# Kernel tuning notes

Hardware: AMD Instinct MI355X
Metric: run time of the kernel (lower is better)

The kernel has to match this reference:

```python
import jax, jax.numpy as jnp
import numpy as np

BATCH, T, IN, OUT, H = 16, 4096, 256, 256, 512


def setup_inputs() -> dict:
    key = jax.random.key(0)
    ks = jax.random.split(key, 8)
    gB = float(np.sqrt(6.0 / (H + IN)))   # glorot uniform bound for B (out_axis=0,in_axis=1)
    gC = float(np.sqrt(6.0 / (OUT + H)))
    gD = float(np.sqrt(6.0 / (OUT + IN)))
    return {
        "X": jax.random.normal(ks[0], (BATCH, T, IN), dtype=jnp.float32),
        "nu_log": jax.random.uniform(ks[1], (H,), dtype=jnp.float32),
        "theta_log": jax.random.uniform(ks[2], (H,), dtype=jnp.float32),
        "B_re": jax.random.uniform(ks[3], (H, IN), jnp.float32, -gB, gB),
        "B_im": jax.random.uniform(ks[4], (H, IN), jnp.float32, -gB, gB),
        "C_re": jax.random.uniform(ks[5], (OUT, H), jnp.float32, -gC, gC),
        "C_im": jax.random.uniform(ks[6], (OUT, H), jnp.float32, -gC, gC),
        "D": jax.random.uniform(ks[7], (OUT, IN), jnp.float32, -gD, gD),
        "bh_re": jnp.zeros((H,), jnp.float32),
        "bh_im": jnp.zeros((H,), jnp.float32),
        "bias_output": jnp.zeros((OUT,), jnp.float32),
    }


def reference(X, nu_log, theta_log, B_re, B_im, C_re, C_im, D, bh_re, bh_im, bias_output):
    # lambda = exp(-exp(nu_log) + i*exp(theta_log)); gamma = sqrt(1-|lambda|^2)
    lam = jnp.exp(-jnp.exp(nu_log) + 1j * jnp.exp(theta_log))          # [H] complex64
    gamma = jnp.sqrt(1.0 - jnp.abs(lam) ** 2)                           # [H] float32
    Bc = (B_re + 1j * B_im).astype(jnp.complex64)
    Cc = (C_re + 1j * C_im).astype(jnp.complex64)
    bh = (bh_re + 1j * bh_im).astype(jnp.complex64)

    # Input projection into hidden space (note: original adds bias_hidden here AND inside the scan step)
    u = gamma * (jnp.einsum('bti,hi->bth', X.astype(jnp.complex64), Bc) + bh)  # [B,T,H] complex64

    def step(h, u_t):
        h = lam * h + u_t + bh
        return h, h

    h0 = jnp.zeros((X.shape[0], lam.shape[0]), dtype=jnp.complex64)
    h_N, ys = jax.lax.scan(step, h0, jnp.swapaxes(u, 0, 1))             # ys: [T,B,H]

    Y = jnp.real(jnp.einsum('tbh,oh->bto', ys, Cc))                     # [B,T,OUT]
    Y = Y + jnp.einsum('bti,oi->bto', X, D) + bias_output
    return (Y, h_N)
```

## Files before the change

kernel.cpp:

```cpp
#include <hip/hip_runtime.h>
#include <math.h>


#define T_LEN  4096
#define NBATCH 16
#define IN_D   256
#define OUT_D  256
#define HID    512
#define M_TOT  65536

typedef __attribute__((ext_vector_type(8))) short short8;
typedef __attribute__((ext_vector_type(4))) float float4v;

static __device__ __forceinline__ unsigned short f2bf(float f) {
    union { float f; unsigned u; } v; v.f = f;
    unsigned r = v.u + 0x7FFFu + ((v.u >> 16) & 1u);
    return (unsigned short)(r >> 16);
}
static __device__ __forceinline__ float bf2f(unsigned short h) {
    union { unsigned u; float f; } v; v.u = ((unsigned)h) << 16;
    return v.f;
}


__global__ __launch_bounds__(256) void cvt_x(const float* __restrict__ X,
                                             unsigned short* __restrict__ Xbf)
{
    int e = (blockIdx.x * 256 + threadIdx.x) * 4;
    float4 v = *(const float4*)(X + e);
    ushort4 o;
    o.x = f2bf(v.x); o.y = f2bf(v.y); o.z = f2bf(v.z); o.w = f2bf(v.w);
    *(ushort4*)(Xbf + e) = o;
}

__global__ __launch_bounds__(256) void cvt_w(
    const float* __restrict__ B_re, const float* __restrict__ B_im,
    const float* __restrict__ C_re, const float* __restrict__ C_im,
    const float* __restrict__ Dm, unsigned short* __restrict__ W)
{
    int e = (blockIdx.x * 256 + threadIdx.x) * 4;
    const float* src; int off;
    if (e < 262144) {
        if (e < 131072) { src = B_re; off = e; }
        else            { src = B_im; off = e - 131072; }
    } else {
        int e2 = e - 262144;
        int row = e2 / 1280, c = e2 % 1280;
        if      (c < 512)  { src = C_re; off = row * 512 + c; }
        else if (c < 1024) { src = C_im; off = row * 512 + c - 512; }
        else               { src = Dm;   off = row * 256 + c - 1024; }
    }
    float4 v = *(const float4*)(src + off);
    ushort4 o;
    o.x = f2bf(v.x); o.y = f2bf(v.y); o.z = f2bf(v.z); o.w = f2bf(v.w);
    *(ushort4*)(W + e) = o;
}

__global__ __launch_bounds__(256) void lam_prep(
    const float* __restrict__ nu_log, const float* __restrict__ theta_log,
    const float* __restrict__ bh_re, float4* __restrict__ Ltab)
{
    int ch = blockIdx.x * 256 + threadIdx.x;
    if (ch >= HID) return;
    float mod = expf(-expf(nu_log[ch]));
    float th  = expf(theta_log[ch]);
    Ltab[ch] = make_float4(mod * cosf(th), mod * sinf(th),
                           sqrtf(fmaxf(0.f, 1.f - mod * mod)), bh_re[ch]);
}

__global__ __launch_bounds__(256, 3) void gemm_scan(
    const unsigned short* __restrict__ Xbf, const unsigned short* __restrict__ Bw,
    const float4* __restrict__ Ltab, const float* __restrict__ bh_im,
    unsigned short* __restrict__ Hbuf, float* __restrict__ hN, int hN_mode)
{
    __shared__ unsigned short smem[160 * 136];

    const int tid  = threadIdx.x;
    const int lane = tid & 63;
    const int wv   = tid >> 6;
    const int wr   = wv >> 1, wc = wv & 1;
    const int col  = lane & 15, quad = lane >> 4;

    const int bid  = blockIdx.x;
    const int xcd  = bid & 7;
    const int idx  = bid >> 3;
    const int chg  = idx & 7;
    const int bc   = xcd * 64 + (idx >> 3);
    const int b    = bc >> 5;
    const int cIdx = bc & 31;

    const int mBase = b * T_LEN + cIdx * 128 - 32;
    const int bLo   = b * T_LEN;

    float4v acc[20];
#pragma unroll
    for (int i = 0; i < 20; ++i) acc[i] = (float4v)0.f;

    int arow[5];
#pragma unroll
    for (int mt = 0; mt < 5; ++mt) {
        int gm = mBase + wr * 80 + mt * 16 + col;
        arow[mt] = gm < bLo ? bLo : gm;
    }
    const unsigned short* Br = Bw + (size_t)(wc * 512 + chg * 64 + col) * IN_D + quad * 8;

#pragma unroll
    for (int ks = 0; ks < 8; ++ks) {
        short8 af[5], bf[4];
#pragma unroll
        for (int mt = 0; mt < 5; ++mt)
            af[mt] = *(const short8*)(Xbf + (size_t)arow[mt] * IN_D + quad * 8 + ks * 32);
#pragma unroll
        for (int nt = 0; nt < 4; ++nt)
            bf[nt] = *(const short8*)(Br + nt * 16 * IN_D + ks * 32);
#pragma unroll
        for (int mt = 0; mt < 5; ++mt)
#pragma unroll
            for (int nt = 0; nt < 4; ++nt)
                acc[mt * 4 + nt] = __builtin_amdgcn_mfma_f32_16x16x32_bf16(
                    af[mt], bf[nt], acc[mt * 4 + nt], 0, 0, 0);
    }

#pragma unroll
    for (int nt = 0; nt < 4; ++nt) {
        const int chl = nt * 16 + col;
        float4 L = Ltab[chg * 64 + chl];
        const float gam = L.z;
        const float bv  = wc ? bh_im[chg * 64 + chl] : L.w;
        const int   cl  = wc * 64 + chl;
#pragma unroll
        for (int mt = 0; mt < 5; ++mt)
#pragma unroll
            for (int r = 0; r < 4; ++r) {
                const int ml = wr * 80 + mt * 16 + quad * 4 + r;
                smem[ml * 136 + cl] = f2bf(gam * (acc[mt * 4 + nt][r] + bv));
            }
    }
    __syncthreads();

    if (wv == 0) {
        float4 L = Ltab[chg * 64 + lane];
        const float lre = L.x, lim = L.y, bre = L.w;
        const float bim = bh_im[chg * 64 + lane];
        float hre = 0.f, him = 0.f;
        const int s0 = (cIdx == 0) ? 32 : 0;
        for (int t0 = s0; t0 < 160; t0 += 8) {
            float ur[8], ui[8];
#pragma unroll
            for (int s = 0; s < 8; ++s) {
                ur[s] = bf2f(smem[(t0 + s) * 136 + lane]);
                ui[s] = bf2f(smem[(t0 + s) * 136 + 64 + lane]);
            }
#pragma unroll
            for (int s = 0; s < 8; ++s) {
                float nr = lre * hre - lim * him + ur[s] + bre;
                him      = lre * him + lim * hre + ui[s] + bim;
                hre = nr;
                smem[(t0 + s) * 136 + lane]      = f2bf(hre);
                smem[(t0 + s) * 136 + 64 + lane] = f2bf(-him);
            }
        }
        if (hN_mode && cIdx == 31) {
            const int ch = chg * 64 + lane;
            if (hN_mode == 2) {
                hN[((size_t)b * HID + ch) * 2]     = hre;
                hN[((size_t)b * HID + ch) * 2 + 1] = him;
            } else {
                hN[(size_t)b * HID + ch] = hre;
            }
        }
    }
    __syncthreads();

    const int p  = tid >> 7;
    const int t7 = tid & 127;
    const int rg = t7 >> 3;
    const int l8 = t7 & 7;
    unsigned short* Hp = Hbuf + ((size_t)(p * 8 + chg) * M_TOT
                                 + (size_t)(b * T_LEN + cIdx * 128)) * 64;
#pragma unroll
    for (int it = 0; it < 8; ++it) {
        const int row = it * 16 + rg;
        short8 v = *(const short8*)(smem + (32 + row) * 136 + p * 64 + l8 * 8);
        *(short8*)(Hp + row * 64 + l8 * 8) = v;
    }
}

__global__ __launch_bounds__(256, 3) void gemm_c(
    const unsigned short* __restrict__ Hbuf, const unsigned short* __restrict__ Xbf,
    const unsigned short* __restrict__ W2,
    const float* __restrict__ bias_out, float* __restrict__ Y)
{
    __shared__ unsigned short sA[128 * 68];
    __shared__ unsigned short sB[128 * 68];
    const int tid  = threadIdx.x;
    const int lane = tid & 63;
    const int wv   = tid >> 6;
    const int wr   = wv >> 1, wc = wv & 1;
    const int col  = lane & 15, quad = lane >> 4;

    const int bid  = blockIdx.x;
    const int xcd  = bid & 7;
    const int idx  = bid >> 3;
    const int Mblk = xcd * 64 + (idx >> 1);
    const int Nblk = idx & 1;
    const int m0 = Mblk * 128, o0 = Nblk * 128;

    float4v acc[16];
#pragma unroll
    for (int i = 0; i < 16; ++i) acc[i] = (float4v)0.f;

    short8 ra[4], rb[4];
#pragma unroll
    for (int i = 0; i < 4; ++i) {
        int cid = i * 256 + tid;
        int r = cid >> 3, c8 = cid & 7;
        ra[i] = *(const short8*)(Hbuf + (size_t)(m0 + r) * 64 + c8 * 8);
        rb[i] = *(const short8*)(W2 + (size_t)(o0 + r) * 1280 + c8 * 8);
    }
    for (int k0 = 0; k0 < 20; ++k0) {
        __syncthreads();
#pragma unroll
        for (int i = 0; i < 4; ++i) {
            int cid = i * 256 + tid;
            int r = cid >> 3, c8 = cid & 7;
            *(short8*)(sA + r * 68 + c8 * 8) = ra[i];
            *(short8*)(sB + r * 68 + c8 * 8) = rb[i];
        }
        __syncthreads();
        if (k0 < 19) {
            const int kn = k0 + 1;
#pragma unroll
            for (int i = 0; i < 4; ++i) {
                int cid = i * 256 + tid;
                int r = cid >> 3, c8 = cid & 7;
                if (kn < 16)
                    ra[i] = *(const short8*)(Hbuf + (size_t)kn * (M_TOT * 64)
                                             + (size_t)(m0 + r) * 64 + c8 * 8);
                else
                    ra[i] = *(const short8*)(Xbf + (size_t)(m0 + r) * 256
                                             + (kn - 16) * 64 + c8 * 8);
                rb[i] = *(const short8*)(W2 + (size_t)(o0 + r) * 1280 + kn * 64 + c8 * 8);
            }
        }
#pragma unroll
        for (int kk = 0; kk < 2; ++kk) {
            short8 af[4], bf[4];
#pragma unroll
            for (int mt = 0; mt < 4; ++mt)
                af[mt] = *(const short8*)(sA + (wr * 64 + mt * 16 + col) * 68 + kk * 32 + quad * 8);
#pragma unroll
            for (int nt = 0; nt < 4; ++nt)
                bf[nt] = *(const short8*)(sB + (wc * 64 + nt * 16 + col) * 68 + kk * 32 + quad * 8);
#pragma unroll
            for (int mt = 0; mt < 4; ++mt)
#pragma unroll
                for (int nt = 0; nt < 4; ++nt)
                    acc[mt * 4 + nt] = __builtin_amdgcn_mfma_f32_16x16x32_bf16(
                        af[mt], bf[nt], acc[mt * 4 + nt], 0, 0, 0);
        }
    }
#pragma unroll
    for (int nt = 0; nt < 4; ++nt) {
        const int o = o0 + wc * 64 + nt * 16 + col;
        const float bo = bias_out[o];
#pragma unroll
        for (int mt = 0; mt < 4; ++mt)
#pragma unroll
            for (int r = 0; r < 4; ++r) {
                const int m = m0 + wr * 64 + mt * 16 + quad * 4 + r;
                Y[(size_t)m * OUT_D + o] = acc[mt * 4 + nt][r] + bo;
            }
    }
}

extern "C" void kernel_launch(void* const* d_in, const int* in_sizes, int n_in,
                              void* d_out, int out_size, void* d_ws, size_t ws_size,
                              hipStream_t stream) {
    const float* X        = (const float*)d_in[0];
    const float* nu_log   = (const float*)d_in[1];
    const float* theta_lg = (const float*)d_in[2];
    const float* B_re     = (const float*)d_in[3];
    const float* B_im     = (const float*)d_in[4];
    const float* C_re     = (const float*)d_in[5];
    const float* C_im     = (const float*)d_in[6];
    const float* Dm       = (const float*)d_in[7];
    const float* bh_re    = (const float*)d_in[8];
    const float* bh_im    = (const float*)d_in[9];
    const float* bias_out = (const float*)d_in[10];

    float* Y = (float*)d_out;
    const int YSZ = NBATCH * T_LEN * OUT_D;
    int extra = out_size - YSZ;
    int mode = (extra >= NBATCH * HID * 2) ? 2 : ((extra >= NBATCH * HID) ? 1 : 0);
    float* hN = Y + YSZ;

    char* ws = (char*)d_ws;
    unsigned short* W    = (unsigned short*)ws;
    unsigned short* W2   = W + 262144;
    float4*         Ltab = (float4*)(ws + 1179648);
    unsigned short* Xbf  = (unsigned short*)(ws + 1187840);
    unsigned short* Hbuf = (unsigned short*)(ws + 34742272);

    cvt_x<<<dim3(16384), 256, 0, stream>>>(X, Xbf);
    cvt_w<<<dim3(576), 256, 0, stream>>>(B_re, B_im, C_re, C_im, Dm, W);
    lam_prep<<<dim3(2), 256, 0, stream>>>(nu_log, theta_lg, bh_re, Ltab);
    gemm_scan<<<dim3(4096), 256, 0, stream>>>(Xbf, W, Ltab, bh_im, Hbuf, hN, mode);
    gemm_c<<<dim3(1024), 256, 0, stream>>>(Hbuf, Xbf, W2, bias_out, Y);
}
```

Before: 360.6 us.

## Halve scan chunk length and use direct global-to-LDS loads in output GEMM

The fused GEMM+scan kernel now processes 64-step time chunks with a 16-step warm-up instead of 128 with 32. It launches twice as many blocks, uses less LDS and fewer accumulators, and raises the occupancy hint. The output GEMM drops its register-staged prefetch and loads tiles straight into LDS with global_load_lds into unpadded tiles. The extra blocks redo more warm-up recurrence and input-projection work, and the unpadded LDS rows plus the lost prefetch overlap may add bank conflicts and stalls.

```diff
diff --git a/kernel.cpp b/kernel.cpp
--- a/kernel.cpp
+++ b/kernel.cpp
@@ -20,6 +20,12 @@
 static __device__ __forceinline__ float bf2f(unsigned short h) {
     union { unsigned u; float f; } v; v.u = ((unsigned)h) << 16;
     return v.f;
+}
+
+static __device__ __forceinline__ void gl_lds16(const void* g, void* l) {
+    __builtin_amdgcn_global_load_lds(
+        (const __attribute__((address_space(1))) unsigned int*)g,
+        (__attribute__((address_space(3))) unsigned int*)l, 16, 0, 0);
 }
 
 
@@ -68,72 +74,74 @@
                            sqrtf(fmaxf(0.f, 1.f - mod * mod)), bh_re[ch]);
 }
 
-__global__ __launch_bounds__(256, 3) void gemm_scan(
+__global__ __launch_bounds__(256, 5) void gemm_scan(
     const unsigned short* __restrict__ Xbf, const unsigned short* __restrict__ Bw,
     const float4* __restrict__ Ltab, const float* __restrict__ bh_im,
     unsigned short* __restrict__ Hbuf, float* __restrict__ hN, int hN_mode)
 {
-    __shared__ unsigned short smem[160 * 136];
+    __shared__ unsigned short smem[80 * 136];
 
     const int tid  = threadIdx.x;
     const int lane = tid & 63;
     const int wv   = tid >> 6;
-    const int wr   = wv >> 1, wc = wv & 1;
     const int col  = lane & 15, quad = lane >> 4;
 
     const int bid  = blockIdx.x;
     const int xcd  = bid & 7;
     const int idx  = bid >> 3;
     const int chg  = idx & 7;
-    const int bc   = xcd * 64 + (idx >> 3);
-    const int b    = bc >> 5;
-    const int cIdx = bc & 31;
-
-    const int mBase = b * T_LEN + cIdx * 128 - 32;
+    const int bcI  = xcd * 128 + (idx >> 3);
+    const int b    = bcI >> 6;
+    const int cIdx = bcI & 63;
+
+    const int mBase = b * T_LEN + cIdx * 64 - 16;
     const int bLo   = b * T_LEN;
 
-    float4v acc[20];
-#pragma unroll
-    for (int i = 0; i < 20; ++i) acc[i] = (float4v)0.f;
+    float4v acc[10];
+#pragma unroll
+    for (int i = 0; i < 10; ++i) acc[i] = (float4v)0.f;
 
     int arow[5];
 #pragma unroll
     for (int mt = 0; mt < 5; ++mt) {
-        int gm = mBase + wr * 80 + mt * 16 + col;
+        int gm = mBase + mt * 16 + col;
         arow[mt] = gm < bLo ? bLo : gm;
     }
-    const unsigned short* Br = Bw + (size_t)(wc * 512 + chg * 64 + col) * IN_D + quad * 8;
+    const int pw = wv >> 1;
+    const int cb = (wv & 1) * 32;
+    const unsigned short* Br =
+        Bw + (size_t)(pw * 512 + chg * 64 + cb + col) * IN_D + quad * 8;
 
 #pragma unroll
     for (int ks = 0; ks < 8; ++ks) {
-        short8 af[5], bf[4];
+        short8 af[5], bf[2];
 #pragma unroll
         for (int mt = 0; mt < 5; ++mt)
             af[mt] = *(const short8*)(Xbf + (size_t)arow[mt] * IN_D + quad * 8 + ks * 32);
 #pragma unroll
-        for (int nt = 0; nt < 4; ++nt)
+        for (int nt = 0; nt < 2; ++nt)
             bf[nt] = *(const short8*)(Br + nt * 16 * IN_D + ks * 32);
 #pragma unroll
         for (int mt = 0; mt < 5; ++mt)
 #pragma unroll
-            for (int nt = 0; nt < 4; ++nt)
-                acc[mt * 4 + nt] = __builtin_amdgcn_mfma_f32_16x16x32_bf16(
-                    af[mt], bf[nt], acc[mt * 4 + nt], 0, 0, 0);
-    }
-
-#pragma unroll
-    for (int nt = 0; nt < 4; ++nt) {
-        const int chl = nt * 16 + col;
+            for (int nt = 0; nt < 2; ++nt)
+                acc[mt * 2 + nt] = __builtin_amdgcn_mfma_f32_16x16x32_bf16(
+                    af[mt], bf[nt], acc[mt * 2 + nt], 0, 0, 0);
+    }
+
+#pragma unroll
+    for (int nt = 0; nt < 2; ++nt) {
+        const int chl = cb + nt * 16 + col;
         float4 L = Ltab[chg * 64 + chl];
         const float gam = L.z;
-        const float bv  = wc ? bh_im[chg * 64 + chl] : L.w;
-        const int   cl  = wc * 64 + chl;
+        const float bv  = pw ? bh_im[chg * 64 + chl] : L.w;
+        const int   cl  = pw * 64 + chl;
 #pragma unroll
         for (int mt = 0; mt < 5; ++mt)
 #pragma unroll
             for (int r = 0; r < 4; ++r) {
-                const int ml = wr * 80 + mt * 16 + quad * 4 + r;
-                smem[ml * 136 + cl] = f2bf(gam * (acc[mt * 4 + nt][r] + bv));
+                const int ml = mt * 16 + quad * 4 + r;
+                smem[ml * 136 + cl] = f2bf(gam * (acc[mt * 2 + nt][r] + bv));
             }
     }
     __syncthreads();
@@ -143,8 +151,8 @@
         const float lre = L.x, lim = L.y, bre = L.w;
         const float bim = bh_im[chg * 64 + lane];
         float hre = 0.f, him = 0.f;
-        const int s0 = (cIdx == 0) ? 32 : 0;
-        for (int t0 = s0; t0 < 160; t0 += 8) {
+        const int s0 = (cIdx == 0) ? 16 : 0;
+        for (int t0 = s0; t0 < 80; t0 += 8) {
             float ur[8], ui[8];
 #pragma unroll
             for (int s = 0; s < 8; ++s) {
@@ -160,7 +168,7 @@
                 smem[(t0 + s) * 136 + 64 + lane] = f2bf(-him);
             }
         }
-        if (hN_mode && cIdx == 31) {
+        if (hN_mode && cIdx == 63) {
             const int ch = chg * 64 + lane;
             if (hN_mode == 2) {
                 hN[((size_t)b * HID + ch) * 2]     = hre;
@@ -177,27 +185,29 @@
     const int rg = t7 >> 3;
     const int l8 = t7 & 7;
     unsigned short* Hp = Hbuf + ((size_t)(p * 8 + chg) * M_TOT
-                                 + (size_t)(b * T_LEN + cIdx * 128)) * 64;
-#pragma unroll
-    for (int it = 0; it < 8; ++it) {
+                                 + (size_t)b * T_LEN + cIdx * 64) * 64;
+#pragma unroll
+    for (int it = 0; it < 4; ++it) {
         const int row = it * 16 + rg;
-        short8 v = *(const short8*)(smem + (32 + row) * 136 + p * 64 + l8 * 8);
+        short8 v = *(const short8*)(smem + (16 + row) * 136 + p * 64 + l8 * 8);
         *(short8*)(Hp + row * 64 + l8 * 8) = v;
     }
 }
 
-__global__ __launch_bounds__(256, 3) void gemm_c(
+__global__ __launch_bounds__(256, 4) void gemm_c(
     const unsigned short* __restrict__ Hbuf, const unsigned short* __restrict__ Xbf,
     const unsigned short* __restrict__ W2,
     const float* __restrict__ bias_out, float* __restrict__ Y)
 {
-    __shared__ unsigned short sA[128 * 68];
-    __shared__ unsigned short sB[128 * 68];
+    __shared__ unsigned short sA[128 * 64];
+    __shared__ unsigned short sB[128 * 64];
     const int tid  = threadIdx.x;
     const int lane = tid & 63;
     const int wv   = tid >> 6;
     const int wr   = wv >> 1, wc = wv & 1;
     const int col  = lane & 15, quad = lane >> 4;
+    const int lr   = lane >> 3;
+    const int lc   = lane & 7;
 
     const int bid  = blockIdx.x;
     const int xcd  = bid & 7;
@@ -210,48 +220,38 @@
 #pragma unroll
     for (int i = 0; i < 16; ++i) acc[i] = (float4v)0.f;
 
-    short8 ra[4], rb[4];
-#pragma unroll
-    for (int i = 0; i < 4; ++i) {
-        int cid = i * 256 + tid;
-        int r = cid >> 3, c8 = cid & 7;
-        ra[i] = *(const short8*)(Hbuf + (size_t)(m0 + r) * 64 + c8 * 8);
-        rb[i] = *(const short8*)(W2 + (size_t)(o0 + r) * 1280 + c8 * 8);
-    }
     for (int k0 = 0; k0 < 20; ++k0) {
         __syncthreads();
 #pragma unroll
-        for (int i = 0; i < 4; ++i) {
-            int cid = i * 256 + tid;
-            int r = cid >> 3, c8 = cid & 7;
-            *(short8*)(sA + r * 68 + c8 * 8) = ra[i];
-            *(short8*)(sB + r * 68 + c8 * 8) = rb[i];
+        for (int c = 0; c < 4; ++c) {
+            const int rr = wv * 32 + c * 8 + lr;
+            const unsigned short* ga;
+            if (k0 < 16)
+                ga = Hbuf + (size_t)k0 * (M_TOT * 64) + (size_t)(m0 + rr) * 64 + lc * 8;
+            else
+                ga = Xbf + (size_t)(m0 + rr) * 256 + (k0 - 16) * 64 + lc * 8;
+            gl_lds16(ga, sA + wv * 2048 + c * 512);
+        }
+#pragma unroll
+        for (int c = 0; c < 4; ++c) {
+            const int rr = wv * 32 + c * 8 + lr;
+            const unsigned short* gb =
+                W2 + (size_t)(o0 + rr) * 1280 + k0 * 64 + lc * 8;
+            gl_lds16(gb, sB + wv * 2048 + c * 512);
         }
         __syncthreads();
-        if (k0 < 19) {
-            const int kn = k0 + 1;
-#pragma unroll
-            for (int i = 0; i < 4; ++i) {
-                int cid = i * 256 + tid;
-                int r = cid >> 3, c8 = cid & 7;
-                if (kn < 16)
-                    ra[i] = *(const short8*)(Hbuf + (size_t)kn * (M_TOT * 64)
-                                             + (size_t)(m0 + r) * 64 + c8 * 8);
-                else
-                    ra[i] = *(const short8*)(Xbf + (size_t)(m0 + r) * 256
-                                             + (kn - 16) * 64 + c8 * 8);
-                rb[i] = *(const short8*)(W2 + (size_t)(o0 + r) * 1280 + kn * 64 + c8 * 8);
-            }
-        }
+
 #pragma unroll
         for (int kk = 0; kk < 2; ++kk) {
             short8 af[4], bf[4];
 #pragma unroll
             for (int mt = 0; mt < 4; ++mt)
-                af[mt] = *(const short8*)(sA + (wr * 64 + mt * 16 + col) * 68 + kk * 32 + quad * 8);
+                af[mt] = *(const short8*)(sA + (wr * 64 + mt * 16 + col) * 64
+                                          + kk * 32 + quad * 8);
 #pragma unroll
             for (int nt = 0; nt < 4; ++nt)
-                bf[nt] = *(const short8*)(sB + (wc * 64 + nt * 16 + col) * 68 + kk * 32 + quad * 8);
+                bf[nt] = *(const short8*)(sB + (wc * 64 + nt * 16 + col) * 64
+                                          + kk * 32 + quad * 8);
 #pragma unroll
             for (int mt = 0; mt < 4; ++mt)
 #pragma unroll
@@ -305,6 +305,6 @@
     cvt_x<<<dim3(16384), 256, 0, stream>>>(X, Xbf);
     cvt_w<<<dim3(576), 256, 0, stream>>>(B_re, B_im, C_re, C_im, Dm, W);
     lam_prep<<<dim3(2), 256, 0, stream>>>(nu_log, theta_lg, bh_re, Ltab);
-    gemm_scan<<<dim3(4096), 256, 0, stream>>>(Xbf, W, Ltab, bh_im, Hbuf, hN, mode);
+    gemm_scan<<<dim3(8192), 256, 0, stream>>>(Xbf, W, Ltab, bh_im, Hbuf, hN, mode);
     gemm_c<<<dim3(1024), 256, 0, stream>>>(Hbuf, Xbf, W2, bias_out, Y);
 }
```

Result: slower. 411.5 us (+14.1%).

## Double-buffer gemm_c via direct global-to-LDS loads with XOR swizzle; prefetch gemm_scan fragments

Applied to the files above, without the earlier changes.

gemm_c now streams A and B tiles straight into a two-stage LDS ring using global_load_lds, with an XOR swizzle in place of row padding. Loads are issued two stages ahead and synchronised with vmcnt waits and barriers, so the register round-trip and one of the two barriers per k-step are gone. gemm_scan register-prefetches the next k-slice of MFMA operands while the current one computes. Occupancy hints drop from 3 to 2 blocks per CU, trading occupancy for more registers and LDS, which risks less latency hiding.

```diff
diff --git a/kernel.cpp b/kernel.cpp
--- a/kernel.cpp
+++ b/kernel.cpp
@@ -20,6 +20,12 @@
 static __device__ __forceinline__ float bf2f(unsigned short h) {
     union { unsigned u; float f; } v; v.u = ((unsigned)h) << 16;
     return v.f;
+}
+
+static __device__ __forceinline__ void gl_lds16(const void* g, void* l) {
+    __builtin_amdgcn_global_load_lds(
+        (const __attribute__((address_space(1))) unsigned int*)g,
+        (__attribute__((address_space(3))) unsigned int*)l, 16, 0, 0);
 }
 
 
@@ -68,7 +74,7 @@
                            sqrtf(fmaxf(0.f, 1.f - mod * mod)), bh_re[ch]);
 }
 
-__global__ __launch_bounds__(256, 3) void gemm_scan(
+__global__ __launch_bounds__(256, 2) void gemm_scan(
     const unsigned short* __restrict__ Xbf, const unsigned short* __restrict__ Bw,
     const float4* __restrict__ Ltab, const float* __restrict__ bh_im,
     unsigned short* __restrict__ Hbuf, float* __restrict__ hN, int hN_mode)
@@ -104,22 +110,36 @@
     }
     const unsigned short* Br = Bw + (size_t)(wc * 512 + chg * 64 + col) * IN_D + quad * 8;
 
+#define LD_A(dst, ks)                                                          \
+    { _Pragma("unroll")                                                        \
+      for (int mt = 0; mt < 5; ++mt)                                           \
+          dst[mt] = *(const short8*)(Xbf + (size_t)arow[mt] * IN_D             \
+                                     + quad * 8 + (ks) * 32); }
+#define LD_B(dst, ks)                                                          \
+    { _Pragma("unroll")                                                        \
+      for (int nt = 0; nt < 4; ++nt)                                           \
+          dst[nt] = *(const short8*)(Br + nt * 16 * IN_D + (ks) * 32); }
+
+    short8 afC[5], bfC[4], afN[5], bfN[4];
+    LD_A(afC, 0) LD_B(bfC, 0)
 #pragma unroll
     for (int ks = 0; ks < 8; ++ks) {
-        short8 af[5], bf[4];
-#pragma unroll
-        for (int mt = 0; mt < 5; ++mt)
-            af[mt] = *(const short8*)(Xbf + (size_t)arow[mt] * IN_D + quad * 8 + ks * 32);
-#pragma unroll
-        for (int nt = 0; nt < 4; ++nt)
-            bf[nt] = *(const short8*)(Br + nt * 16 * IN_D + ks * 32);
+        if (ks < 7) { LD_A(afN, ks + 1) LD_B(bfN, ks + 1) }
 #pragma unroll
         for (int mt = 0; mt < 5; ++mt)
 #pragma unroll
             for (int nt = 0; nt < 4; ++nt)
                 acc[mt * 4 + nt] = __builtin_amdgcn_mfma_f32_16x16x32_bf16(
-                    af[mt], bf[nt], acc[mt * 4 + nt], 0, 0, 0);
-    }
+                    afC[mt], bfC[nt], acc[mt * 4 + nt], 0, 0, 0);
+        if (ks < 7) {
+#pragma unroll
+            for (int mt = 0; mt < 5; ++mt) afC[mt] = afN[mt];
+#pragma unroll
+            for (int nt = 0; nt < 4; ++nt) bfC[nt] = bfN[nt];
+        }
+    }
+#undef LD_A
+#undef LD_B
 
 #pragma unroll
     for (int nt = 0; nt < 4; ++nt) {
@@ -177,7 +197,7 @@
     const int rg = t7 >> 3;
     const int l8 = t7 & 7;
     unsigned short* Hp = Hbuf + ((size_t)(p * 8 + chg) * M_TOT
-                                 + (size_t)(b * T_LEN + cIdx * 128)) * 64;
+                                 + (size_t)b * T_LEN + cIdx * 128) * 64;
 #pragma unroll
     for (int it = 0; it < 8; ++it) {
         const int row = it * 16 + rg;
@@ -186,18 +206,21 @@
     }
 }
 
-__global__ __launch_bounds__(256, 3) void gemm_c(
+__global__ __launch_bounds__(256, 2) void gemm_c(
     const unsigned short* __restrict__ Hbuf, const unsigned short* __restrict__ Xbf,
     const unsigned short* __restrict__ W2,
     const float* __restrict__ bias_out, float* __restrict__ Y)
 {
-    __shared__ unsigned short sA[128 * 68];
-    __shared__ unsigned short sB[128 * 68];
+    __shared__ unsigned short sA[2][128 * 64];
+    __shared__ unsigned short sB[2][128 * 64];
     const int tid  = threadIdx.x;
     const int lane = tid & 63;
     const int wv   = tid >> 6;
     const int wr   = wv >> 1, wc = wv & 1;
     const int col  = lane & 15, quad = lane >> 4;
+    const int lr   = lane >> 3;
+    const int lc   = lane & 7;
+    const int lcS  = lc ^ lr;
 
     const int bid  = blockIdx.x;
     const int xcd  = bid & 7;
@@ -210,48 +233,52 @@
 #pragma unroll
     for (int i = 0; i < 16; ++i) acc[i] = (float4v)0.f;
 
-    short8 ra[4], rb[4];
-#pragma unroll
-    for (int i = 0; i < 4; ++i) {
-        int cid = i * 256 + tid;
-        int r = cid >> 3, c8 = cid & 7;
-        ra[i] = *(const short8*)(Hbuf + (size_t)(m0 + r) * 64 + c8 * 8);
-        rb[i] = *(const short8*)(W2 + (size_t)(o0 + r) * 1280 + c8 * 8);
-    }
+#define STAGE(p, k0)                                                           \
+    {                                                                          \
+        _Pragma("unroll")                                                      \
+        for (int c = 0; c < 4; ++c) {                                          \
+            const int rr = wv * 32 + c * 8 + lr;                               \
+            const unsigned short* ga;                                          \
+            if ((k0) < 16)                                                     \
+                ga = Hbuf + (size_t)(k0) * ((size_t)M_TOT * 64)                \
+                     + (size_t)(m0 + rr) * 64 + lcS * 8;                       \
+            else                                                               \
+                ga = Xbf + (size_t)(m0 + rr) * 256 + ((k0) - 16) * 64 + lcS * 8; \
+            gl_lds16(ga, &sA[p][wv * 2048 + c * 512]);                         \
+        }                                                                      \
+        _Pragma("unroll")                                                      \
+        for (int c = 0; c < 4; ++c) {                                          \
+            const int rr = wv * 32 + c * 8 + lr;                               \
+            gl_lds16(W2 + (size_t)(o0 + rr) * 1280 + (k0) * 64 + lcS * 8,      \
+                     &sB[p][wv * 2048 + c * 512]);                             \
+        }                                                                      \
+    }
+
+    STAGE(0, 0)
+    STAGE(1, 1)
+
     for (int k0 = 0; k0 < 20; ++k0) {
-        __syncthreads();
-#pragma unroll
-        for (int i = 0; i < 4; ++i) {
-            int cid = i * 256 + tid;
-            int r = cid >> 3, c8 = cid & 7;
-            *(short8*)(sA + r * 68 + c8 * 8) = ra[i];
-            *(short8*)(sB + r * 68 + c8 * 8) = rb[i];
-        }
-        __syncthreads();
-        if (k0 < 19) {
-            const int kn = k0 + 1;
-#pragma unroll
-            for (int i = 0; i < 4; ++i) {
-                int cid = i * 256 + tid;
-                int r = cid >> 3, c8 = cid & 7;
-                if (kn < 16)
-                    ra[i] = *(const short8*)(Hbuf + (size_t)kn * (M_TOT * 64)
-                                             + (size_t)(m0 + r) * 64 + c8 * 8);
-                else
-                    ra[i] = *(const short8*)(Xbf + (size_t)(m0 + r) * 256
-                                             + (kn - 16) * 64 + c8 * 8);
-                rb[i] = *(const short8*)(W2 + (size_t)(o0 + r) * 1280 + kn * 64 + c8 * 8);
-            }
-        }
+        const int p = k0 & 1;
+        if (k0 < 19) { asm volatile("s_waitcnt vmcnt(8)" ::: "memory"); }
+        else         { asm volatile("s_waitcnt vmcnt(0)" ::: "memory"); }
+        __builtin_amdgcn_s_barrier();
+        __builtin_amdgcn_sched_barrier(0);
+
 #pragma unroll
         for (int kk = 0; kk < 2; ++kk) {
             short8 af[4], bf[4];
 #pragma unroll
-            for (int mt = 0; mt < 4; ++mt)
-                af[mt] = *(const short8*)(sA + (wr * 64 + mt * 16 + col) * 68 + kk * 32 + quad * 8);
-#pragma unroll
-            for (int nt = 0; nt < 4; ++nt)
-                bf[nt] = *(const short8*)(sB + (wc * 64 + nt * 16 + col) * 68 + kk * 32 + quad * 8);
+            for (int mt = 0; mt < 4; ++mt) {
+                const int row = wr * 64 + mt * 16 + col;
+                af[mt] = *(const short8*)(&sA[p][(row * 64 + kk * 32 + quad * 8)
+                                                 ^ ((row & 7) << 3)]);
+            }
+#pragma unroll
+            for (int nt = 0; nt < 4; ++nt) {
+                const int row = wc * 64 + nt * 16 + col;
+                bf[nt] = *(const short8*)(&sB[p][(row * 64 + kk * 32 + quad * 8)
+                                                 ^ ((row & 7) << 3)]);
+            }
 #pragma unroll
             for (int mt = 0; mt < 4; ++mt)
 #pragma unroll
@@ -259,7 +286,14 @@
                     acc[mt * 4 + nt] = __builtin_amdgcn_mfma_f32_16x16x32_bf16(
                         af[mt], bf[nt], acc[mt * 4 + nt], 0, 0, 0);
         }
-    }
+
+        __builtin_amdgcn_sched_barrier(0);
+        __builtin_amdgcn_s_barrier();
+        __builtin_amdgcn_sched_barrier(0);
+        if (k0 < 18) STAGE(p, k0 + 2)
+    }
+#undef STAGE
+
 #pragma unroll
     for (int nt = 0; nt < 4; ++nt) {
         const int o = o0 + wc * 64 + nt * 16 + col;
```

Measured after the change: 397.7 us. +10.3%, slower.

## Fuse X conversion, input GEMM, chunked scan and output GEMM into one kernel

Applied to the files above, without the earlier changes.

Replaces the separate X conversion, gemm_scan and gemm_c kernels with a single kernel that converts a 96-row X tile to bf16 in shared memory, computes the B projection per 64-channel group, runs the truncated-warmup scan in LDS, and immediately accumulates the C and D projections into register-held Y tiles. This removes the global round trip of the bf16 X copy and the large hidden-state buffer, plus two launches. In exchange each block redoes the 32-step warmup window per channel group with 64-step chunks (more redundant GEMM and scan work), has lower occupancy, and the scan is split across four waves that each recompute a 32-step warmup.

```diff
diff --git a/kernel.cpp b/kernel.cpp
--- a/kernel.cpp
+++ b/kernel.cpp
@@ -8,6 +8,8 @@
 #define OUT_D  256
 #define HID    512
 #define M_TOT  65536
+#define XT_STR 264
+#define HT_STR 136
 
 typedef __attribute__((ext_vector_type(8))) short short8;
 typedef __attribute__((ext_vector_type(4))) float float4v;
@@ -22,16 +24,6 @@
     return v.f;
 }
 
-
-__global__ __launch_bounds__(256) void cvt_x(const float* __restrict__ X,
-                                             unsigned short* __restrict__ Xbf)
-{
-    int e = (blockIdx.x * 256 + threadIdx.x) * 4;
-    float4 v = *(const float4*)(X + e);
-    ushort4 o;
-    o.x = f2bf(v.x); o.y = f2bf(v.y); o.z = f2bf(v.z); o.w = f2bf(v.w);
-    *(ushort4*)(Xbf + e) = o;
-}
 
 __global__ __launch_bounds__(256) void cvt_w(
     const float* __restrict__ B_re, const float* __restrict__ B_im,
@@ -68,100 +60,128 @@
                            sqrtf(fmaxf(0.f, 1.f - mod * mod)), bh_re[ch]);
 }
 
-__global__ __launch_bounds__(256, 3) void gemm_scan(
-    const unsigned short* __restrict__ Xbf, const unsigned short* __restrict__ Bw,
+__global__ __launch_bounds__(256, 2) void lru_mega(
+    const float* __restrict__ X, const unsigned short* __restrict__ Bw,
+    const unsigned short* __restrict__ W2,
     const float4* __restrict__ Ltab, const float* __restrict__ bh_im,
-    unsigned short* __restrict__ Hbuf, float* __restrict__ hN, int hN_mode)
+    const float* __restrict__ bias_out,
+    float* __restrict__ Y, float* __restrict__ hN, int hN_mode)
 {
-    __shared__ unsigned short smem[160 * 136];
+    __shared__ unsigned short Xt[96 * XT_STR];
+    __shared__ unsigned short Ht[96 * HT_STR];
 
     const int tid  = threadIdx.x;
     const int lane = tid & 63;
     const int wv   = tid >> 6;
+    const int col  = lane & 15, quad = lane >> 4;
     const int wr   = wv >> 1, wc = wv & 1;
-    const int col  = lane & 15, quad = lane >> 4;
 
     const int bid  = blockIdx.x;
     const int xcd  = bid & 7;
-    const int idx  = bid >> 3;
-    const int chg  = idx & 7;
-    const int bc   = xcd * 64 + (idx >> 3);
-    const int b    = bc >> 5;
-    const int cIdx = bc & 31;
-
-    const int mBase = b * T_LEN + cIdx * 128 - 32;
-    const int bLo   = b * T_LEN;
-
-    float4v acc[20];
-#pragma unroll
-    for (int i = 0; i < 20; ++i) acc[i] = (float4v)0.f;
-
-    int arow[5];
-#pragma unroll
-    for (int mt = 0; mt < 5; ++mt) {
-        int gm = mBase + wr * 80 + mt * 16 + col;
-        arow[mt] = gm < bLo ? bLo : gm;
-    }
-    const unsigned short* Br = Bw + (size_t)(wc * 512 + chg * 64 + col) * IN_D + quad * 8;
-
-#pragma unroll
-    for (int ks = 0; ks < 8; ++ks) {
-        short8 af[5], bf[4];
-#pragma unroll
-        for (int mt = 0; mt < 5; ++mt)
-            af[mt] = *(const short8*)(Xbf + (size_t)arow[mt] * IN_D + quad * 8 + ks * 32);
-#pragma unroll
-        for (int nt = 0; nt < 4; ++nt)
-            bf[nt] = *(const short8*)(Br + nt * 16 * IN_D + ks * 32);
-#pragma unroll
-        for (int mt = 0; mt < 5; ++mt)
+    const int bc   = xcd * 128 + (bid >> 3);
+    const int b    = bc >> 6;
+    const int cIdx = bc & 63;
+    const int G0   = b * T_LEN + cIdx * 64;
+    const int bLo  = b * T_LEN;
+
+#pragma unroll 4
+    for (int i = 0; i < 24; ++i) {
+        const int r = wv * 24 + i;
+        int g = G0 - 32 + r; if (g < bLo) g = bLo;
+        float4 v = *(const float4*)(X + (size_t)g * IN_D + lane * 4);
+        ushort4 o;
+        o.x = f2bf(v.x); o.y = f2bf(v.y); o.z = f2bf(v.z); o.w = f2bf(v.w);
+        *(ushort4*)(Xt + r * XT_STR + lane * 4) = o;
+    }
+    __syncthreads();
+
+    float4v yac[16];
+#pragma unroll
+    for (int i = 0; i < 16; ++i) yac[i] = (float4v)0.f;
+
+    for (int p = 0; p < 8; ++p) {
+        float4v ua[12];
+#pragma unroll
+        for (int i = 0; i < 12; ++i) ua[i] = (float4v)0.f;
+        const unsigned short* Brow =
+            Bw + (size_t)(wc * 512 + p * 64 + col) * IN_D + quad * 8;
+#pragma unroll
+        for (int ks = 0; ks < 8; ++ks) {
+            short8 af[3], bf[4];
+#pragma unroll
+            for (int mt = 0; mt < 3; ++mt)
+                af[mt] = *(const short8*)(Xt + (wr * 48 + mt * 16 + col) * XT_STR
+                                          + ks * 32 + quad * 8);
 #pragma unroll
             for (int nt = 0; nt < 4; ++nt)
-                acc[mt * 4 + nt] = __builtin_amdgcn_mfma_f32_16x16x32_bf16(
-                    af[mt], bf[nt], acc[mt * 4 + nt], 0, 0, 0);
-    }
-
-#pragma unroll
-    for (int nt = 0; nt < 4; ++nt) {
-        const int chl = nt * 16 + col;
-        float4 L = Ltab[chg * 64 + chl];
-        const float gam = L.z;
-        const float bv  = wc ? bh_im[chg * 64 + chl] : L.w;
-        const int   cl  = wc * 64 + chl;
-#pragma unroll
-        for (int mt = 0; mt < 5; ++mt)
-#pragma unroll
-            for (int r = 0; r < 4; ++r) {
-                const int ml = wr * 80 + mt * 16 + quad * 4 + r;
-                smem[ml * 136 + cl] = f2bf(gam * (acc[mt * 4 + nt][r] + bv));
-            }
-    }
-    __syncthreads();
-
-    if (wv == 0) {
-        float4 L = Ltab[chg * 64 + lane];
+                bf[nt] = *(const short8*)(Brow + nt * 16 * IN_D + ks * 32);
+#pragma unroll
+            for (int mt = 0; mt < 3; ++mt)
+#pragma unroll
+                for (int nt = 0; nt < 4; ++nt)
+                    ua[mt * 4 + nt] = __builtin_amdgcn_mfma_f32_16x16x32_bf16(
+                        af[mt], bf[nt], ua[mt * 4 + nt], 0, 0, 0);
+        }
+        __syncthreads();
+
+#pragma unroll
+        for (int nt = 0; nt < 4; ++nt) {
+            const int chl = nt * 16 + col;
+            const int ch  = p * 64 + chl;
+            float4 L = Ltab[ch];
+            const float gam = L.z;
+            const float bv  = wc ? bh_im[ch] : L.w;
+            const int   cl  = wc * 64 + chl;
+#pragma unroll
+            for (int mt = 0; mt < 3; ++mt)
+#pragma unroll
+                for (int r = 0; r < 4; ++r) {
+                    const int ml = wr * 48 + mt * 16 + quad * 4 + r;
+                    Ht[ml * HT_STR + cl] = f2bf(gam * (ua[mt * 4 + nt][r] + bv));
+                }
+        }
+        __syncthreads();
+
+        float4 L = Ltab[p * 64 + lane];
         const float lre = L.x, lim = L.y, bre = L.w;
-        const float bim = bh_im[chg * 64 + lane];
+        const float bim = bh_im[p * 64 + lane];
         float hre = 0.f, him = 0.f;
-        const int s0 = (cIdx == 0) ? 32 : 0;
-        for (int t0 = s0; t0 < 160; t0 += 8) {
+        const int outBeg  = 32 + 16 * wv;
+        const int warmBeg = (cIdx == 0) ? 32 : (outBeg - 32);
+        for (int t0 = warmBeg; t0 < outBeg; t0 += 8) {
             float ur[8], ui[8];
 #pragma unroll
             for (int s = 0; s < 8; ++s) {
-                ur[s] = bf2f(smem[(t0 + s) * 136 + lane]);
-                ui[s] = bf2f(smem[(t0 + s) * 136 + 64 + lane]);
+                ur[s] = bf2f(Ht[(t0 + s) * HT_STR + lane]);
+                ui[s] = bf2f(Ht[(t0 + s) * HT_STR + 64 + lane]);
             }
 #pragma unroll
             for (int s = 0; s < 8; ++s) {
                 float nr = lre * hre - lim * him + ur[s] + bre;
                 him      = lre * him + lim * hre + ui[s] + bim;
                 hre = nr;
-                smem[(t0 + s) * 136 + lane]      = f2bf(hre);
-                smem[(t0 + s) * 136 + 64 + lane] = f2bf(-him);
-            }
-        }
-        if (hN_mode && cIdx == 31) {
-            const int ch = chg * 64 + lane;
+            }
+        }
+        __syncthreads();
+#pragma unroll
+        for (int t0 = outBeg; t0 < outBeg + 16; t0 += 8) {
+            float ur[8], ui[8];
+#pragma unroll
+            for (int s = 0; s < 8; ++s) {
+                ur[s] = bf2f(Ht[(t0 + s) * HT_STR + lane]);
+                ui[s] = bf2f(Ht[(t0 + s) * HT_STR + 64 + lane]);
+            }
+#pragma unroll
+            for (int s = 0; s < 8; ++s) {
+                float nr = lre * hre - lim * him + ur[s] + bre;
+                him      = lre * him + lim * hre + ui[s] + bim;
+                hre = nr;
+                Ht[(t0 + s) * HT_STR + lane]      = f2bf(hre);
+                Ht[(t0 + s) * HT_STR + 64 + lane] = f2bf(-him);
+            }
+        }
+        if (hN_mode && cIdx == 63 && wv == 3) {
+            const int ch = p * 64 + lane;
             if (hN_mode == 2) {
                 hN[((size_t)b * HID + ch) * 2]     = hre;
                 hN[((size_t)b * HID + ch) * 2 + 1] = him;
@@ -169,107 +189,61 @@
                 hN[(size_t)b * HID + ch] = hre;
             }
         }
-    }
-    __syncthreads();
-
-    const int p  = tid >> 7;
-    const int t7 = tid & 127;
-    const int rg = t7 >> 3;
-    const int l8 = t7 & 7;
-    unsigned short* Hp = Hbuf + ((size_t)(p * 8 + chg) * M_TOT
-                                 + (size_t)(b * T_LEN + cIdx * 128)) * 64;
-#pragma unroll
-    for (int it = 0; it < 8; ++it) {
-        const int row = it * 16 + rg;
-        short8 v = *(const short8*)(smem + (32 + row) * 136 + p * 64 + l8 * 8);
-        *(short8*)(Hp + row * 64 + l8 * 8) = v;
-    }
-}
-
-__global__ __launch_bounds__(256, 3) void gemm_c(
-    const unsigned short* __restrict__ Hbuf, const unsigned short* __restrict__ Xbf,
-    const unsigned short* __restrict__ W2,
-    const float* __restrict__ bias_out, float* __restrict__ Y)
-{
-    __shared__ unsigned short sA[128 * 68];
-    __shared__ unsigned short sB[128 * 68];
-    const int tid  = threadIdx.x;
-    const int lane = tid & 63;
-    const int wv   = tid >> 6;
-    const int wr   = wv >> 1, wc = wv & 1;
-    const int col  = lane & 15, quad = lane >> 4;
-
-    const int bid  = blockIdx.x;
-    const int xcd  = bid & 7;
-    const int idx  = bid >> 3;
-    const int Mblk = xcd * 64 + (idx >> 1);
-    const int Nblk = idx & 1;
-    const int m0 = Mblk * 128, o0 = Nblk * 128;
-
-    float4v acc[16];
-#pragma unroll
-    for (int i = 0; i < 16; ++i) acc[i] = (float4v)0.f;
-
-    short8 ra[4], rb[4];
-#pragma unroll
-    for (int i = 0; i < 4; ++i) {
-        int cid = i * 256 + tid;
-        int r = cid >> 3, c8 = cid & 7;
-        ra[i] = *(const short8*)(Hbuf + (size_t)(m0 + r) * 64 + c8 * 8);
-        rb[i] = *(const short8*)(W2 + (size_t)(o0 + r) * 1280 + c8 * 8);
-    }
-    for (int k0 = 0; k0 < 20; ++k0) {
-        __syncthreads();
-#pragma unroll
-        for (int i = 0; i < 4; ++i) {
-            int cid = i * 256 + tid;
-            int r = cid >> 3, c8 = cid & 7;
-            *(short8*)(sA + r * 68 + c8 * 8) = ra[i];
-            *(short8*)(sB + r * 68 + c8 * 8) = rb[i];
-        }
-        __syncthreads();
-        if (k0 < 19) {
-            const int kn = k0 + 1;
-#pragma unroll
-            for (int i = 0; i < 4; ++i) {
-                int cid = i * 256 + tid;
-                int r = cid >> 3, c8 = cid & 7;
-                if (kn < 16)
-                    ra[i] = *(const short8*)(Hbuf + (size_t)kn * (M_TOT * 64)
-                                             + (size_t)(m0 + r) * 64 + c8 * 8);
-                else
-                    ra[i] = *(const short8*)(Xbf + (size_t)(m0 + r) * 256
-                                             + (kn - 16) * 64 + c8 * 8);
-                rb[i] = *(const short8*)(W2 + (size_t)(o0 + r) * 1280 + kn * 64 + c8 * 8);
-            }
-        }
-#pragma unroll
-        for (int kk = 0; kk < 2; ++kk) {
-            short8 af[4], bf[4];
-#pragma unroll
-            for (int mt = 0; mt < 4; ++mt)
-                af[mt] = *(const short8*)(sA + (wr * 64 + mt * 16 + col) * 68 + kk * 32 + quad * 8);
+        __syncthreads();
+
+        const unsigned short* Wrow = W2 + (size_t)(wv * 64 + col) * 1280 + quad * 8;
+#pragma unroll
+        for (int half = 0; half < 2; ++half) {
+#pragma unroll
+            for (int kk = 0; kk < 2; ++kk) {
+                short8 af[4], bf[4];
+#pragma unroll
+                for (int mt = 0; mt < 4; ++mt)
+                    af[mt] = *(const short8*)(Ht + (32 + mt * 16 + col) * HT_STR
+                                              + half * 64 + kk * 32 + quad * 8);
+#pragma unroll
+                for (int nt = 0; nt < 4; ++nt)
+                    bf[nt] = *(const short8*)(Wrow + nt * 16 * 1280
+                                              + half * 512 + p * 64 + kk * 32);
+#pragma unroll
+                for (int mt = 0; mt < 4; ++mt)
+#pragma unroll
+                    for (int nt = 0; nt < 4; ++nt)
+                        yac[mt * 4 + nt] = __builtin_amdgcn_mfma_f32_16x16x32_bf16(
+                            af[mt], bf[nt], yac[mt * 4 + nt], 0, 0, 0);
+            }
+        }
+    }
+
+    const unsigned short* WrowD = W2 + (size_t)(wv * 64 + col) * 1280 + 1024 + quad * 8;
+#pragma unroll
+    for (int ks = 0; ks < 8; ++ks) {
+        short8 af[4], bf[4];
+#pragma unroll
+        for (int mt = 0; mt < 4; ++mt)
+            af[mt] = *(const short8*)(Xt + (32 + mt * 16 + col) * XT_STR
+                                      + ks * 32 + quad * 8);
+#pragma unroll
+        for (int nt = 0; nt < 4; ++nt)
+            bf[nt] = *(const short8*)(WrowD + nt * 16 * 1280 + ks * 32);
+#pragma unroll
+        for (int mt = 0; mt < 4; ++mt)
 #pragma unroll
             for (int nt = 0; nt < 4; ++nt)
-                bf[nt] = *(const short8*)(sB + (wc * 64 + nt * 16 + col) * 68 + kk * 32 + quad * 8);
-#pragma unroll
-            for (int mt = 0; mt < 4; ++mt)
-#pragma unroll
-                for (int nt = 0; nt < 4; ++nt)
-                    acc[mt * 4 + nt] = __builtin_amdgcn_mfma_f32_16x16x32_bf16(
-                        af[mt], bf[nt], acc[mt * 4 + nt], 0, 0, 0);
-        }
-    }
+                yac[mt * 4 + nt] = __builtin_amdgcn_mfma_f32_16x16x32_bf16(
+                    af[mt], bf[nt], yac[mt * 4 + nt], 0, 0, 0);
+    }
+
 #pragma unroll
     for (int nt = 0; nt < 4; ++nt) {
-        const int o = o0 + wc * 64 + nt * 16 + col;
+        const int o = wv * 64 + nt * 16 + col;
         const float bo = bias_out[o];
 #pragma unroll
         for (int mt = 0; mt < 4; ++mt)
 #pragma unroll
             for (int r = 0; r < 4; ++r) {
-                const int m = m0 + wr * 64 + mt * 16 + quad * 4 + r;
-                Y[(size_t)m * OUT_D + o] = acc[mt * 4 + nt][r] + bo;
+                const int m = G0 + mt * 16 + quad * 4 + r;
+                Y[(size_t)m * OUT_D + o] = yac[mt * 4 + nt][r] + bo;
             }
     }
 }
@@ -299,12 +273,9 @@
     unsigned short* W    = (unsigned short*)ws;
     unsigned short* W2   = W + 262144;
     float4*         Ltab = (float4*)(ws + 1179648);
-    unsigned short* Xbf  = (unsigned short*)(ws + 1187840);
-    unsigned short* Hbuf = (unsigned short*)(ws + 34742272);
-
-    cvt_x<<<dim3(16384), 256, 0, stream>>>(X, Xbf);
+
     cvt_w<<<dim3(576), 256, 0, stream>>>(B_re, B_im, C_re, C_im, Dm, W);
     lam_prep<<<dim3(2), 256, 0, stream>>>(nu_log, theta_lg, bh_re, Ltab);
-    gemm_scan<<<dim3(4096), 256, 0, stream>>>(Xbf, W, Ltab, bh_im, Hbuf, hN, mode);
-    gemm_c<<<dim3(1024), 256, 0, stream>>>(Hbuf, Xbf, W2, bias_out, Y);
-}
+    lru_mega<<<dim3(1024), 256, 0, stream>>>(X, W, W2, Ltab, bh_im, bias_out,
+                                             Y, hN, mode);
+}
```

Result: no change. 361.0 us (+0.1%).
